# Kernel tuning notes

Measured on AMD Instinct MI355X. Metric: run time of the kernel, lower is better.

## Reference

```python
import jax, jax.numpy as jnp
import numpy as np

B, C, D, H, W = 8, 96, 8, 32, 32
HW, DIM, NH = H * W, C * D, 4
DH = DIM // NH
EPS_NORM = 1e-12
EPS_LN = 1e-5


def setup_inputs() -> dict:
    key = jax.random.key(0)
    ks = jax.random.split(key, 10)
    s = 0.02
    return {
        "x": jax.random.normal(ks[0], (B, C, D, H, W), jnp.float32),
        "pos_embed": jax.random.normal(ks[1], (1, HW, DIM), jnp.float32) * s,
        "qkv_w": jax.random.normal(ks[2], (3 * DIM, DIM), jnp.float32) * s,
        "proj_w": jax.random.normal(ks[3], (DIM, DIM), jnp.float32) * s,
        "proj_b": jnp.zeros((DIM,), jnp.float32),
        "temperature": jnp.ones((NH, 1, 1), jnp.float32),
        "ln_gamma": jnp.ones((DIM,), jnp.float32),
        "ln_beta": jnp.zeros((DIM,), jnp.float32),
        "dw_w": jax.random.normal(ks[4], (C, 1, 3, 3, 3), jnp.float32) * s,
        "dw_b": jnp.zeros((C,), jnp.float32),
        "pw_w": jax.random.normal(ks[5], (C, C, 1, 1, 1), jnp.float32) * s,
        "pw_b": jnp.zeros((C,), jnp.float32),
    }


def _l2norm_seq(t):
    # normalize over the HW axis (dim=-2), matching F.normalize(dim=-2)
    n = jnp.sqrt(jnp.sum(t * t, axis=-2, keepdims=True))
    return t / jnp.maximum(n, EPS_NORM)


def _dsconv(y, dw_w, dw_b, pw_w, pw_b):
    dn = ("NCDHW", "OIDHW", "NCDHW")
    z = jax.lax.conv_general_dilated(y, dw_w, (1, 1, 1), [(1, 1)] * 3,
                                     dimension_numbers=dn, feature_group_count=C)
    z = z + dw_b[None, :, None, None, None]
    z = jax.lax.conv_general_dilated(z, pw_w, (1, 1, 1), [(0, 0)] * 3,
                                     dimension_numbers=dn)
    return z + pw_b[None, :, None, None, None]


def reference(x, pos_embed, qkv_w, proj_w, proj_b, temperature,
              ln_gamma, ln_beta, dw_w, dw_b, pw_w, pw_b):
    save = x
    # b c d h w -> b (h w) (c d)
    t = jnp.transpose(x, (0, 3, 4, 1, 2)).reshape(B, HW, DIM)
    t = t + pos_embed
    # qkv projection (no bias)
    qkv = (t @ qkv_w.T).reshape(B, HW, 3, NH, DH)
    qkv = jnp.transpose(qkv, (2, 0, 3, 1, 4))  # [3,B,NH,HW,DH]
    q, k, v = qkv[0], qkv[1], qkv[2]
    q = _l2norm_seq(q)
    k = _l2norm_seq(k)
    attn = jnp.einsum("bhnd,bhmd->bhnm", q, k) * temperature  # temp broadcasts [NH,1,1]
    attn = jax.nn.softmax(attn, axis=-1)  # dropout = identity at eval
    o = jnp.einsum("bhnm,bhmd->bhnd", attn, v)
    o = jnp.transpose(o, (0, 2, 1, 3)).reshape(B, HW, DIM)
    o = o @ proj_w.T + proj_b
    # LayerNorm applied to attention output
    mu = jnp.mean(o, axis=-1, keepdims=True)
    var = jnp.mean((o - mu) ** 2, axis=-1, keepdims=True)
    o = (o - mu) / jnp.sqrt(var + EPS_LN) * ln_gamma + ln_beta
    # b (h w) (c d) -> b c d h w
    o = o.reshape(B, H, W, C, D)
    o = jnp.transpose(o, (0, 3, 4, 1, 2))
    y = o + save
    return y + _dsconv(y, dw_w, dw_b, pw_w, pw_b)
```

## Files before the change

### kernel.cpp

```cpp
#include <hip/hip_runtime.h>

typedef unsigned short u16;
typedef unsigned int u32;

typedef __attribute__((ext_vector_type(8))) short short8;
typedef __attribute__((ext_vector_type(4))) float floatx4;

__device__ __forceinline__ float bf2f(u16 u) { return __uint_as_float(((u32)u) << 16); }
__device__ __forceinline__ u16 f2bf(float f) {
    u32 x = __float_as_uint(f);
    x += 0x7fffu + ((x >> 16) & 1u);
    return (u16)(x >> 16);
}
__device__ __forceinline__ void gl_lds16(const void* g, void* l) {
    __builtin_amdgcn_global_load_lds((const __attribute__((address_space(1))) u32*)g,
                                     (__attribute__((address_space(3))) u32*)l, 16, 0, 0);
}


__global__ __launch_bounds__(256) void k_init(const float* __restrict__ x,
                                              const float* __restrict__ pos,
                                              const float* __restrict__ wq,
                                              const float* __restrict__ wp,
                                              const float* __restrict__ wpw,
                                              u16* __restrict__ t,
                                              u16* __restrict__ wout,
                                              float* __restrict__ zbuf) {
    __shared__ float tile[64][65];
    const int bid = blockIdx.x;
    const int tid = threadIdx.x;
    if (bid < 1536) {
        const int cd0 = (bid % 12) * 64;
        const int hw0 = ((bid / 12) & 15) * 64;
        const int b = bid / 192;
#pragma unroll
        for (int i = 0; i < 16; i++) {
            int f = i * 256 + tid;
            int cdl = f >> 6, hwl = f & 63;
            int cd = cd0 + cdl, c = cd >> 3, d = cd & 7;
            tile[cdl][hwl] = x[(size_t)(((b * 96 + c) * 8 + d)) * 1024 + hw0 + hwl];
        }
        __syncthreads();
#pragma unroll
        for (int it = 0; it < 2; it++) {
            int u = it * 256 + tid;
            int ch = u >> 6, l = u & 63;
            int n16l = ch >> 1, kcl = ch & 1;
            int hwl = n16l * 16 + (l & 15);
            int cdl = kcl * 32 + (l >> 4) * 8;
            int row = b * 1024 + hw0 + hwl;
            int cd = cd0 + cdl;
            const float* pp = pos + (size_t)(hw0 + hwl) * 768 + cd;
            float4 p0 = *(const float4*)pp;
            float4 p1 = *(const float4*)(pp + 4);
            short8 v;
            v[0] = (short)f2bf(tile[cdl + 0][hwl] + p0.x);
            v[1] = (short)f2bf(tile[cdl + 1][hwl] + p0.y);
            v[2] = (short)f2bf(tile[cdl + 2][hwl] + p0.z);
            v[3] = (short)f2bf(tile[cdl + 3][hwl] + p0.w);
            v[4] = (short)f2bf(tile[cdl + 4][hwl] + p1.x);
            v[5] = (short)f2bf(tile[cdl + 5][hwl] + p1.y);
            v[6] = (short)f2bf(tile[cdl + 6][hwl] + p1.z);
            v[7] = (short)f2bf(tile[cdl + 7][hwl] + p1.w);
            size_t chunk = (size_t)(row >> 4) * 24 + (cd >> 5);
            *(short8*)(t + chunk * 512 + l * 8) = v;
        }
    } else if (bid < 2724) {
        const int NQ = 144 * 24 * 64;
        const int NP = NQ + 48 * 24 * 64;
        int u = (bid - 1536) * 256 + tid;
        if (u < NP) {
            const float* w = (u < NQ) ? wq : wp;
            int ub = (u < NQ) ? u : u - NQ;
            int chunk = ub >> 6, l = ub & 63;
            int n16 = chunk / 24, kc = chunk - n16 * 24;
            int n = n16 * 16 + (l & 15);
            int k0 = kc * 32 + (l >> 4) * 8;
            const float* src = w + (size_t)n * 768 + k0;
            float4 a = *(const float4*)src;
            float4 b2 = *(const float4*)(src + 4);
            short8 v;
            v[0] = (short)f2bf(a.x);  v[1] = (short)f2bf(a.y);
            v[2] = (short)f2bf(a.z);  v[3] = (short)f2bf(a.w);
            v[4] = (short)f2bf(b2.x); v[5] = (short)f2bf(b2.y);
            v[6] = (short)f2bf(b2.z); v[7] = (short)f2bf(b2.w);
            *(short8*)(wout + (size_t)u * 8) = v;
        } else {
            int i = u - NP;
            wout[(size_t)NP * 8 + i] = f2bf(wpw[i]);
        }
    } else {
        int i = (bid - 2724) * 256 + tid;
        zbuf[i] = 0.f;
    }
}

template <int MODE>
__global__ __launch_bounds__(256) void gemm_bt(const u16* __restrict__ A,
                                               const u16* __restrict__ Bw,
                                               int M, int N, int K,
                                               u16* __restrict__ qo, u16* __restrict__ ko,
                                               u16* __restrict__ vo,
                                               const float* __restrict__ bias,
                                               u16* __restrict__ Co,
                                               float* __restrict__ sqa,
                                               float* __restrict__ ska,
                                               float* __restrict__ musum,
                                               float* __restrict__ sqsum) {
    __shared__ __align__(16) u16 lAB[128 * 136];
    u16* lA = lAB;
    u16* lB = lAB + 16 * 512;
    const int tid = threadIdx.x;
    const int lane = tid & 63;
    const int wv = tid >> 6;
    const int wr = wv >> 1, wc = wv & 1;
    const int ntiles = N >> 7;
    const int mtiles = M >> 7;
    const int lin = blockIdx.x;
    const int xcd = lin & 7;
    const int idx = lin >> 3;
    const int mlocal = idx / ntiles;
    const int ntile = idx - mlocal * ntiles;
    const int m0 = (xcd * (mtiles >> 3) + mlocal) << 7;
    const int n0 = ntile << 7;
    const int lr = lane & 15;
    const int lq = lane >> 4;

    floatx4 acc[4][4];
#pragma unroll
    for (int i = 0; i < 4; i++)
#pragma unroll
        for (int j = 0; j < 4; j++) acc[i][j] = (floatx4){0.f, 0.f, 0.f, 0.f};

    const int m16 = m0 >> 4, n16 = n0 >> 4;
    for (int kc2 = 0; kc2 < (K >> 6); kc2++) {
        __syncthreads();
#pragma unroll
        for (int kh = 0; kh < 2; kh++) {
#pragma unroll
            for (int i = 0; i < 2; i++) {
                int ch16 = i * 4 + wv;
                int kc = kc2 * 2 + kh;
                const u16* ga = A + ((size_t)(m16 + ch16) * 24 + kc) * 512 + lane * 8;
                gl_lds16(ga, (char*)lA + (kh * 8 + ch16) * 1024);
                const u16* gb = Bw + ((size_t)(n16 + ch16) * 24 + kc) * 512 + lane * 8;
                gl_lds16(gb, (char*)lB + (kh * 8 + ch16) * 1024);
            }
        }
        __syncthreads();
#pragma unroll
        for (int kh = 0; kh < 2; kh++) {
            short8 af[4], bfr[4];
#pragma unroll
            for (int tt = 0; tt < 4; tt++) {
                af[tt] = *(const short8*)(lA + ((kh * 8 + wr * 4 + tt) * 64 + lane) * 8);
                bfr[tt] = *(const short8*)(lB + ((kh * 8 + wc * 4 + tt) * 64 + lane) * 8);
            }
#pragma unroll
            for (int mt = 0; mt < 4; mt++)
#pragma unroll
                for (int nt = 0; nt < 4; nt++)
                    acc[mt][nt] = __builtin_amdgcn_mfma_f32_16x16x32_bf16(af[mt], bfr[nt], acc[mt][nt], 0, 0, 0);
        }
    }

    if (MODE == 0) {
        const int region = n0 / 768;
        const int n0r = n0 - region * 768;
        const int bb0 = m0 >> 10;
        if (region < 2) {
            float* dst = (region == 0) ? sqa : ska;
#pragma unroll
            for (int nt = 0; nt < 4; nt++) {
                int colb = n0r + wc * 64 + nt * 16;
                int h = colb / 192;
                int dh = colb - h * 192 + lr;
                float s = 0.f;
#pragma unroll
                for (int mt = 0; mt < 4; mt++)
#pragma unroll
                    for (int r = 0; r < 4; r++) s += acc[mt][nt][r] * acc[mt][nt][r];
                s += __shfl_xor(s, 16);
                s += __shfl_xor(s, 32);
                if (lq == 0) atomicAdd(&dst[(bb0 * 4 + h) * 192 + dh], s);
            }
        }
        __syncthreads();
        if (region < 2) {
#pragma unroll
            for (int nt = 0; nt < 4; nt++) {
                int lch = wc * 2 + (nt >> 1);
                int offbase = (((nt & 1) * 2 + (lr >> 3)) * 16) * 8 + (lr & 7);
#pragma unroll
                for (int mt = 0; mt < 4; mt++) {
                    u16* cp2 = lAB + (((wr * 4 + mt) * 4 + lch) * 512);
#pragma unroll
                    for (int r = 0; r < 4; r++)
                        cp2[offbase + (lq * 4 + r) * 8] = f2bf(acc[mt][nt][r]);
                }
            }
        } else {
#pragma unroll
            for (int nt = 0; nt < 4; nt++) {
#pragma unroll
                for (int mt = 0; mt < 4; mt++) {
                    u16* cp2 = lAB + (((wr * 2 + (mt >> 1)) * 8 + wc * 4 + nt) * 512);
                    int ob = (((mt & 1) * 2 + (lq >> 1)) * 16 + lr) * 8 + (lq & 1) * 4;
#pragma unroll
                    for (int r = 0; r < 4; r++)
                        cp2[ob + r] = f2bf(acc[mt][nt][r]);
                }
            }
        }
        __syncthreads();
        const int b = m0 >> 10;
        const int ml = m0 & 1023;
        u16* dsto = (region == 0) ? qo : (region == 1) ? ko : vo;
#pragma unroll
        for (int i = 0; i < 8; i++) {
            int ci = wv * 8 + i;
            short8 val = *(const short8*)(lAB + ci * 512 + lane * 8);
            if (region < 2) {
                int a = ci >> 2, bb = ci & 3;
                int cg = n0r + bb * 32;
                int h = cg / 192;
                int dh32 = (cg - h * 192) >> 5;
                size_t gaddr = (size_t)(b * 4 + h) * 196608 +
                               (size_t)((((ml >> 4) + a) * 6 + dh32)) * 512 + lane * 8;
                *(short8*)(dsto + gaddr) = val;
            } else {
                int a = ci >> 3, bb = ci & 7;
                int cg = n0r + bb * 16;
                int h = cg / 192;
                int dh16 = (cg - h * 192) >> 4;
                size_t gaddr = (size_t)(b * 4 + h) * 196608 +
                               (size_t)((((ml >> 5) + a) * 12 + dh16)) * 512 + lane * 8;
                *(short8*)(dsto + gaddr) = val;
            }
        }
    } else {
        float bvv[4];
#pragma unroll
        for (int nt = 0; nt < 4; nt++) bvv[nt] = bias[n0 + wc * 64 + nt * 16 + lr];
#pragma unroll
        for (int mt = 0; mt < 4; mt++) {
#pragma unroll
            for (int r = 0; r < 4; r++) {
                float s = 0.f, ss = 0.f;
#pragma unroll
                for (int nt = 0; nt < 4; nt++) {
                    float v = acc[mt][nt][r] + bvv[nt];
                    s += v;
                    ss += v * v;
                }
#pragma unroll
                for (int m = 1; m < 16; m <<= 1) {
                    s += __shfl_xor(s, m);
                    ss += __shfl_xor(ss, m);
                }
                if (lr == 0) {
                    int row = m0 + wr * 64 + mt * 16 + lq * 4 + r;
                    atomicAdd(&musum[row], s);
                    atomicAdd(&sqsum[row], ss);
                }
            }
        }
        __syncthreads();
#pragma unroll
        for (int nt = 0; nt < 4; nt++) {
            int coll = wc * 64 + nt * 16 + lr;
#pragma unroll
            for (int mt = 0; mt < 4; mt++) {
#pragma unroll
                for (int r = 0; r < 4; r++) {
                    int rowl = wr * 64 + mt * 16 + lq * 4 + r;
                    lAB[rowl * 136 + coll] = f2bf(acc[mt][nt][r] + bvv[nt]);
                }
            }
        }
        __syncthreads();
#pragma unroll
        for (int i = 0; i < 8; i++) {
            int u = i * 256 + tid;
            int rowl = u >> 4, l = u & 15;
            short8 val = *(const short8*)(lAB + rowl * 136 + l * 8);
            *(short8*)(Co + (size_t)(m0 + rowl) * N + n0 + l * 8) = val;
        }
    }
}

__global__ __launch_bounds__(256) void k_attn(const u16* __restrict__ q,
                                              const u16* __restrict__ kmat,
                                              const u16* __restrict__ vT,
                                              const float* __restrict__ sqq,
                                              const float* __restrict__ sqk,
                                              const float* __restrict__ temp,
                                              u16* __restrict__ o) {
    __shared__ __align__(16) u16 lK[24 * 512];
    __shared__ __align__(16) u16 lV[24 * 512];
    __shared__ __align__(16) u16 lP[4 * 1024];
    __shared__ float lcs[192];
    const int lin = blockIdx.x;
    const int qb = (lin >> 3) & 15;
    const int bh = (lin & 7) * 4 + (lin >> 7);
    const int b = bh >> 2, h = bh & 3;
    const int tid = threadIdx.x;
    const int lane = tid & 63;
    const int wv = tid >> 6;
    const int lr = lane & 15;
    const int lq = lane >> 4;
    const int koff = lq * 8;

    const u16* qbase = q + (size_t)bh * 196608;
    const u16* kbase = kmat + (size_t)bh * 196608;
    const u16* vbase = vT + (size_t)bh * 196608;

    {
        const float tv = temp[bh & 3];
        for (int i = tid; i < 192; i += 256) {
            float rq = 1.f / fmaxf(sqrtf(sqq[bh * 192 + i]), 1e-12f);
            float rk = 1.f / fmaxf(sqrtf(sqk[bh * 192 + i]), 1e-12f);
            lcs[i] = rq * rk * tv;
        }
    }
    __syncthreads();

    short8 qf[6];
    {
        const int qr16 = qb * 4 + wv;
#pragma unroll
        for (int ks = 0; ks < 6; ks++) {
            short8 raw = *(const short8*)(qbase + ((size_t)(qr16 * 6 + ks)) * 512 + (size_t)lane * 8);
            short8 sc;
#pragma unroll
            for (int j = 0; j < 8; j++) {
                float f = bf2f((u16)raw[j]) * lcs[ks * 32 + koff + j];
                sc[j] = (short)f2bf(f);
            }
            qf[ks] = sc;
        }
    }

    float l_r[4];
    floatx4 oacc[12];
#pragma unroll
    for (int r = 0; r < 4; r++) l_r[r] = 0.f;
#pragma unroll
    for (int vt = 0; vt < 12; vt++) oacc[vt] = (floatx4){0.f, 0.f, 0.f, 0.f};

    u16* lp = lP + wv * 1024;

    auto stage_K = [&](int kb2) {
#pragma unroll
        for (int i = 0; i < 6; i++) {
            int ch = i * 4 + wv;
            int ks = ch >> 2, nt = ch & 3;
            const u16* gk = kbase + ((size_t)(kb2 * 4 + nt) * 6 + ks) * 512 + lane * 8;
            gl_lds16(gk, (char*)lK + ch * 1024);
        }
    };
    auto stage_V = [&](int kb2) {
#pragma unroll
        for (int i = 0; i < 6; i++) {
            int ch = i * 4 + wv;
            int ks2 = ch / 12, vt2 = ch - ks2 * 12;
            const u16* gv = vbase + ((size_t)(kb2 * 2 + ks2) * 12 + vt2) * 512 + lane * 8;
            gl_lds16(gv, (char*)lV + ch * 1024);
        }
    };

    asm volatile("s_waitcnt vmcnt(0)" ::: "memory");
    stage_K(0);
    stage_V(0);
    asm volatile("s_waitcnt vmcnt(6)" ::: "memory");
    __builtin_amdgcn_s_barrier();

    for (int kb = 0; kb < 16; kb++) {
        floatx4 s0[4];
#pragma unroll
        for (int nt = 0; nt < 4; nt++) s0[nt] = (floatx4){0.f, 0.f, 0.f, 0.f};
        __builtin_amdgcn_s_setprio(1);
#pragma unroll
        for (int ks = 0; ks < 6; ks++) {
#pragma unroll
            for (int nt = 0; nt < 4; nt++) {
                short8 kf = *(const short8*)(lK + ((ks * 4 + nt) * 64 + lane) * 8);
                s0[nt] = __builtin_amdgcn_mfma_f32_16x16x32_bf16(qf[ks], kf, s0[nt], 0, 0, 0);
            }
        }
        __builtin_amdgcn_s_setprio(0);
        __builtin_amdgcn_s_barrier();
        if (kb < 15) stage_K(kb + 1);

        float rs0[4] = {0.f, 0.f, 0.f, 0.f};
#pragma unroll
        for (int nt = 0; nt < 4; nt++)
#pragma unroll
            for (int r = 0; r < 4; r++) {
                float p0 = __expf(s0[nt][r]);
                s0[nt][r] = p0;
                rs0[r] += p0;
            }
#pragma unroll
        for (int m = 1; m < 16; m <<= 1)
#pragma unroll
            for (int r = 0; r < 4; r++) rs0[r] += __shfl_xor(rs0[r], m);
#pragma unroll
        for (int r = 0; r < 4; r++) l_r[r] += rs0[r];
#pragma unroll
        for (int nt = 0; nt < 4; nt++) {
            int base2 = (nt >> 1) * 512 + ((nt & 1) * 2 + (lr >> 3)) * 128 + (lr & 7);
#pragma unroll
            for (int r = 0; r < 4; r++)
                lp[base2 + (lq * 4 + r) * 8] = f2bf(s0[nt][r]);
        }

        if (kb < 15) { asm volatile("s_waitcnt vmcnt(6)" ::: "memory"); }
        else         { asm volatile("s_waitcnt vmcnt(0)" ::: "memory"); }
        __builtin_amdgcn_s_barrier();

        __builtin_amdgcn_s_setprio(1);
#pragma unroll
        for (int ks2 = 0; ks2 < 2; ks2++) {
            short8 pf0 = *(const short8*)(lp + ks2 * 512 + lane * 8);
#pragma unroll
            for (int vt = 0; vt < 12; vt++) {
                short8 vf = *(const short8*)(lV + ((ks2 * 12 + vt) * 64 + lane) * 8);
                oacc[vt] = __builtin_amdgcn_mfma_f32_16x16x32_bf16(pf0, vf, oacc[vt], 0, 0, 0);
            }
        }
        __builtin_amdgcn_s_setprio(0);
        __builtin_amdgcn_s_barrier();
        if (kb < 15) {
            stage_V(kb + 1);
            asm volatile("s_waitcnt vmcnt(6)" ::: "memory");
            __builtin_amdgcn_s_barrier();
        }
    }

    __syncthreads();
    {
        float inv[4];
#pragma unroll
        for (int r = 0; r < 4; r++) inv[r] = 1.f / l_r[r];
#pragma unroll
        for (int vt = 0; vt < 12; vt++) {
            int col = vt * 16 + lr;
            int swb = (col >> 5) * 512 + (((col >> 3) & 3) * 16) * 8 + (col & 7);
#pragma unroll
            for (int r = 0; r < 4; r++) {
                int rowl = wv * 16 + lq * 4 + r;
                lK[(rowl >> 4) * 3072 + swb + (rowl & 15) * 8] = f2bf(oacc[vt][r] * inv[r]);
            }
        }
    }
    __syncthreads();
#pragma unroll
    for (int i = 0; i < 6; i++) {
        int u = i * 256 + tid;
        int chl = u >> 6, l = u & 63;
        short8 val = *(const short8*)(lK + chl * 512 + l * 8);
        int a = chl / 6, kc = chl - a * 6;
        size_t gaddr = ((size_t)(b * 64 + qb * 4 + a) * 24 + h * 6 + kc) * 512 + l * 8;
        *(short8*)(o + gaddr) = val;
    }
}

__global__ __launch_bounds__(256) void k_lnt(const u16* __restrict__ o2,
                                             const float* __restrict__ musum,
                                             const float* __restrict__ sqsum,
                                             const float* __restrict__ gamma,
                                             const float* __restrict__ beta,
                                             const float* __restrict__ x,
                                             float* __restrict__ y) {
    __shared__ float tile[64][65];
    const int b = blockIdx.z, hw0 = blockIdx.y * 64, cd0 = blockIdx.x * 64;
    const int tid = threadIdx.x;
#pragma unroll
    for (int i = 0; i < 16; i++) {
        int f = i * 256 + tid;
        int hwl = f >> 6, cdl = f & 63;
        int row = b * 1024 + hw0 + hwl;
        float m_ = musum[row] * (1.f / 768.f);
        float var = fmaxf(sqsum[row] * (1.f / 768.f) - m_ * m_, 0.f);
        float rstd = rsqrtf(var + 1e-5f);
        float v = bf2f(o2[(size_t)row * 768 + cd0 + cdl]);
        v = (v - m_) * rstd * gamma[cd0 + cdl] + beta[cd0 + cdl];
        tile[hwl][cdl] = v;
    }
    __syncthreads();
#pragma unroll
    for (int i = 0; i < 16; i++) {
        int f = i * 256 + tid;
        int cdl = f >> 6, hwl = f & 63;
        int cd = cd0 + cdl, c = cd >> 3, d = cd & 7;
        size_t addr = (size_t)((b * 96 + c) * 8 + d) * 1024 + hw0 + hwl;
        y[addr] = tile[hwl][cdl] + x[addr];
    }
}

__global__ __launch_bounds__(256) void k_dw(const float* __restrict__ y,
                                            const float* __restrict__ w,
                                            const float* __restrict__ bias,
                                            u16* __restrict__ z) {
    __shared__ float ly[8192];
    const int bc = blockIdx.x;
    const int c = bc % 96;
    const int tid = threadIdx.x;
    const size_t base = (size_t)bc * 8192;

#pragma unroll
    for (int i = 0; i < 8; i++) {
        int i4 = i * 256 + tid;
        *(float4*)(ly + i4 * 4) = *(const float4*)(y + base + i4 * 4);
    }
    float wt[27];
#pragma unroll
    for (int j = 0; j < 27; j++) wt[j] = w[c * 27 + j];
    const float bv = bias[c];
    __syncthreads();

    const int wcol = tid & 31;
    const int hh = tid >> 5;

    for (int hb = 0; hb < 4; hb++) {
        const int h = hb * 8 + hh;
        float pl[3][9];
        auto loadplane = [&](int dd, float* p) {
#pragma unroll
            for (int kh = 0; kh < 3; kh++) {
                int h2 = h + kh - 1;
                bool hok = (unsigned)h2 < 32u;
                const float* row = ly + dd * 1024 + h2 * 32;
#pragma unroll
                for (int kw = 0; kw < 3; kw++) {
                    int w2 = wcol + kw - 1;
                    bool ok = hok && (unsigned)w2 < 32u;
                    p[kh * 3 + kw] = ok ? row[w2] : 0.f;
                }
            }
        };
#pragma unroll
        for (int j = 0; j < 9; j++) pl[0][j] = 0.f;
        loadplane(0, pl[1]);
#pragma unroll
        for (int d = 0; d < 8; d++) {
            if (d < 7) loadplane(d + 1, pl[2]);
            else {
#pragma unroll
                for (int j = 0; j < 9; j++) pl[2][j] = 0.f;
            }
            float acc = bv;
#pragma unroll
            for (int kd = 0; kd < 3; kd++)
#pragma unroll
                for (int j = 0; j < 9; j++) acc += wt[kd * 9 + j] * pl[kd][j];
            z[base + d * 1024 + h * 32 + wcol] = f2bf(acc);
#pragma unroll
            for (int j = 0; j < 9; j++) { pl[0][j] = pl[1][j]; pl[1][j] = pl[2][j]; }
        }
    }
}

__global__ __launch_bounds__(256) void k_pw(const u16* __restrict__ z,
                                            const u16* __restrict__ wbf,
                                            const float* __restrict__ bias,
                                            float* __restrict__ out) {
    __shared__ __align__(16) u16 lZ[128 * 104];
    __shared__ __align__(16) u16 lW[96 * 104];
    const int tid = threadIdx.x;
    const int lane = tid & 63;
    const int wv = tid >> 6;
    const int lr = lane & 15;
    const int lq = lane >> 4;
    const int koff = lq * 8;

    const int idx = blockIdx.x;
    const int q = idx & 7;
    const int bd = idx >> 3;
    const int b = bd >> 3, d = bd & 7;
    const int pos0 = q * 128;

    for (int i = tid; i < 96 * 96; i += 256) {
        int row = i / 96, col = i - row * 96;
        lW[row * 104 + col] = wbf[i];
    }
    {
        const int pos = tid & 127;
        const int cc0 = (tid >> 7) * 48;
        const size_t gbase = ((size_t)b * 96 * 8 + d) * 1024 + pos0 + pos;
#pragma unroll
        for (int g = 0; g < 6; g++) {
            short8 v;
#pragma unroll
            for (int j = 0; j < 8; j++) {
                int cc = cc0 + g * 8 + j;
                v[j] = (short)z[gbase + (size_t)cc * 8192];
            }
            *(short8*)(lZ + pos * 104 + cc0 + g * 8) = v;
        }
    }
    __syncthreads();

    floatx4 acc[6][2];
#pragma unroll
    for (int m = 0; m < 6; m++)
#pragma unroll
        for (int nt = 0; nt < 2; nt++) acc[m][nt] = (floatx4){0.f, 0.f, 0.f, 0.f};

#pragma unroll
    for (int ks = 0; ks < 3; ks++) {
        short8 bfrg[2];
#pragma unroll
        for (int nt = 0; nt < 2; nt++)
            bfrg[nt] = *(const short8*)(lZ + (wv * 32 + nt * 16 + lr) * 104 + ks * 32 + koff);
#pragma unroll
        for (int m = 0; m < 6; m++) {
            short8 afr = *(const short8*)(lW + (m * 16 + lr) * 104 + ks * 32 + koff);
#pragma unroll
            for (int nt = 0; nt < 2; nt++)
                acc[m][nt] = __builtin_amdgcn_mfma_f32_16x16x32_bf16(afr, bfrg[nt], acc[m][nt], 0, 0, 0);
        }
    }

#pragma unroll
    for (int m = 0; m < 6; m++) {
#pragma unroll
        for (int r = 0; r < 4; r++) {
            int c = m * 16 + lq * 4 + r;
            float bv = bias[c];
            size_t rowbase = ((size_t)(b * 96 + c) * 8 + d) * 1024 + pos0;
#pragma unroll
            for (int nt = 0; nt < 2; nt++) {
                int pos = wv * 32 + nt * 16 + lr;
                size_t a = rowbase + pos;
                out[a] = out[a] + bv + acc[m][nt][r];
            }
        }
    }
}

extern "C" void kernel_launch(void* const* d_in, const int* in_sizes, int n_in,
                              void* d_out, int out_size, void* d_ws, size_t ws_size,
                              hipStream_t stream) {
    (void)in_sizes; (void)n_in; (void)out_size; (void)ws_size;
    const float* x      = (const float*)d_in[0];
    const float* pos    = (const float*)d_in[1];
    const float* qkv_w  = (const float*)d_in[2];
    const float* proj_w = (const float*)d_in[3];
    const float* proj_b = (const float*)d_in[4];
    const float* temp   = (const float*)d_in[5];
    const float* ln_g   = (const float*)d_in[6];
    const float* ln_b   = (const float*)d_in[7];
    const float* dw_w   = (const float*)d_in[8];
    const float* dw_b   = (const float*)d_in[9];
    const float* pw_w   = (const float*)d_in[10];
    const float* pw_b   = (const float*)d_in[11];
    float* out = (float*)d_out;
    char* ws = (char*)d_ws;

    u16* t    = (u16*)(ws + 0);
    u16* vT   = (u16*)(ws + 12582912);
    u16* q    = (u16*)(ws + 25165824);
    u16* kk   = (u16*)(ws + 37748736);
    u16* wqb  = (u16*)(ws + 50331648);
    float* sqq   = (float*)(ws + 55175168);
    float* sqk   = (float*)(ws + 55199744);
    float* musum = (float*)(ws + 55224320);
    float* sqsum = (float*)(ws + 55257088);
    u16* wpb  = wqb + 2304 * 768;
    u16* wpwb = wqb + 2304 * 768 + 768 * 768;
    u16* o   = t;
    u16* o2  = q;
    u16* z   = t;
    float* y  = out;

    k_init<<<2836, 256, 0, stream>>>(x, pos, qkv_w, proj_w, pw_w, t, wqb, sqq);
    gemm_bt<0><<<1152, 256, 0, stream>>>(t, wqb, 8192, 2304, 768, q, kk, vT, nullptr, nullptr,
                                         sqq, sqk, nullptr, nullptr);
    k_attn<<<512, 256, 0, stream>>>(q, kk, vT, sqq, sqk, temp, o);
    gemm_bt<1><<<384, 256, 0, stream>>>(o, wpb, 8192, 768, 768, nullptr, nullptr, nullptr, proj_b,
                                        o2, nullptr, nullptr, musum, sqsum);
    k_lnt<<<dim3(12, 16, 8), 256, 0, stream>>>(o2, musum, sqsum, ln_g, ln_b, x, y);
    k_dw<<<768, 256, 0, stream>>>(y, dw_w, dw_b, z);
    k_pw<<<512, 256, 0, stream>>>(z, wpwb, pw_b, out);
}
```

Before: 251.1 us.

## Split attention key blocks across wave pairs and double attention grid size

Each attention block now handles 32 query rows instead of 64, with the four waves arranged as 2 row groups by 2 key-column halves. Each wave computes scores for half of each key tile, and the partial outputs and row sums of the two waves in a pair are combined through shared memory at the end. The grid doubles from 512 to 1024 blocks, which raises occupancy and parallelism across CUs. The cost is that each block reloads the full K and V tiles for half as many queries, doubling global K/V traffic, and the cross-wave reduction adds extra LDS work and barriers. The lcs scratch array is also aliased onto the smaller P buffer.

```diff
diff --git a/kernel.cpp b/kernel.cpp
--- a/kernel.cpp
+++ b/kernel.cpp
@@ -298,15 +298,17 @@
                                               u16* __restrict__ o) {
     __shared__ __align__(16) u16 lK[24 * 512];
     __shared__ __align__(16) u16 lV[24 * 512];
-    __shared__ __align__(16) u16 lP[4 * 1024];
-    __shared__ float lcs[192];
+    __shared__ __align__(16) u16 lP[4 * 512];
+    float* lcs = (float*)lP;
     const int lin = blockIdx.x;
-    const int qb = (lin >> 3) & 15;
-    const int bh = (lin & 7) * 4 + (lin >> 7);
+    const int qb = (lin >> 3) & 31;
+    const int bh = (lin & 7) * 4 + (lin >> 8);
     const int b = bh >> 2, h = bh & 3;
     const int tid = threadIdx.x;
     const int lane = tid & 63;
     const int wv = tid >> 6;
+    const int wrow = wv >> 1;
+    const int wcol = wv & 1;
     const int lr = lane & 15;
     const int lq = lane >> 4;
     const int koff = lq * 8;
@@ -327,7 +329,7 @@
 
     short8 qf[6];
     {
-        const int qr16 = qb * 4 + wv;
+        const int qr16 = qb * 2 + wrow;
 #pragma unroll
         for (int ks = 0; ks < 6; ks++) {
             short8 raw = *(const short8*)(qbase + ((size_t)(qr16 * 6 + ks)) * 512 + (size_t)lane * 8);
@@ -348,7 +350,7 @@
 #pragma unroll
     for (int vt = 0; vt < 12; vt++) oacc[vt] = (floatx4){0.f, 0.f, 0.f, 0.f};
 
-    u16* lp = lP + wv * 1024;
+    u16* lp = lP + wv * 512;
 
     auto stage_K = [&](int kb2) {
 #pragma unroll
@@ -376,15 +378,15 @@
     __builtin_amdgcn_s_barrier();
 
     for (int kb = 0; kb < 16; kb++) {
-        floatx4 s0[4];
-#pragma unroll
-        for (int nt = 0; nt < 4; nt++) s0[nt] = (floatx4){0.f, 0.f, 0.f, 0.f};
+        floatx4 s0[2];
+#pragma unroll
+        for (int nt = 0; nt < 2; nt++) s0[nt] = (floatx4){0.f, 0.f, 0.f, 0.f};
         __builtin_amdgcn_s_setprio(1);
 #pragma unroll
         for (int ks = 0; ks < 6; ks++) {
 #pragma unroll
-            for (int nt = 0; nt < 4; nt++) {
-                short8 kf = *(const short8*)(lK + ((ks * 4 + nt) * 64 + lane) * 8);
+            for (int nt = 0; nt < 2; nt++) {
+                short8 kf = *(const short8*)(lK + ((ks * 4 + wcol * 2 + nt) * 64 + lane) * 8);
                 s0[nt] = __builtin_amdgcn_mfma_f32_16x16x32_bf16(qf[ks], kf, s0[nt], 0, 0, 0);
             }
         }
@@ -394,7 +396,7 @@
 
         float rs0[4] = {0.f, 0.f, 0.f, 0.f};
 #pragma unroll
-        for (int nt = 0; nt < 4; nt++)
+        for (int nt = 0; nt < 2; nt++)
 #pragma unroll
             for (int r = 0; r < 4; r++) {
                 float p0 = __expf(s0[nt][r]);
@@ -408,8 +410,8 @@
 #pragma unroll
         for (int r = 0; r < 4; r++) l_r[r] += rs0[r];
 #pragma unroll
-        for (int nt = 0; nt < 4; nt++) {
-            int base2 = (nt >> 1) * 512 + ((nt & 1) * 2 + (lr >> 3)) * 128 + (lr & 7);
+        for (int nt = 0; nt < 2; nt++) {
+            int base2 = (nt * 2 + (lr >> 3)) * 128 + (lr & 7);
 #pragma unroll
             for (int r = 0; r < 4; r++)
                 lp[base2 + (lq * 4 + r) * 8] = f2bf(s0[nt][r]);
@@ -420,12 +422,11 @@
         __builtin_amdgcn_s_barrier();
 
         __builtin_amdgcn_s_setprio(1);
-#pragma unroll
-        for (int ks2 = 0; ks2 < 2; ks2++) {
-            short8 pf0 = *(const short8*)(lp + ks2 * 512 + lane * 8);
+        {
+            short8 pf0 = *(const short8*)(lp + lane * 8);
 #pragma unroll
             for (int vt = 0; vt < 12; vt++) {
-                short8 vf = *(const short8*)(lV + ((ks2 * 12 + vt) * 64 + lane) * 8);
+                short8 vf = *(const short8*)(lV + ((wcol * 12 + vt) * 64 + lane) * 8);
                 oacc[vt] = __builtin_amdgcn_mfma_f32_16x16x32_bf16(pf0, vf, oacc[vt], 0, 0, 0);
             }
         }
@@ -439,29 +440,55 @@
     }
 
     __syncthreads();
+    float lfull[4];
+    {
+        u16* base = (wv < 2) ? lK : lV;
+        float* mine = (float*)(base + (wv & 1) * 6144);
+#pragma unroll
+        for (int vt = 0; vt < 12; vt++)
+#pragma unroll
+            for (int r = 0; r < 4; r++) mine[(vt * 64 + lane) * 4 + r] = oacc[vt][r];
+        if (lr == 0) {
+            float* Lw = (float*)lP + wv * 16;
+#pragma unroll
+            for (int r = 0; r < 4; r++) Lw[lq * 4 + r] = l_r[r];
+        }
+        __syncthreads();
+        const float* theirs = (const float*)(base + ((wv & 1) ^ 1) * 6144);
+        const float* Lp = (const float*)lP + (wv ^ 1) * 16;
+#pragma unroll
+        for (int vt = 0; vt < 12; vt++)
+#pragma unroll
+            for (int r = 0; r < 4; r++) oacc[vt][r] += theirs[(vt * 64 + lane) * 4 + r];
+#pragma unroll
+        for (int r = 0; r < 4; r++) lfull[r] = l_r[r] + Lp[lq * 4 + r];
+    }
+    __syncthreads();
+
     {
         float inv[4];
 #pragma unroll
-        for (int r = 0; r < 4; r++) inv[r] = 1.f / l_r[r];
-#pragma unroll
-        for (int vt = 0; vt < 12; vt++) {
+        for (int r = 0; r < 4; r++) inv[r] = 1.f / lfull[r];
+#pragma unroll
+        for (int i = 0; i < 6; i++) {
+            int vt = wcol * 6 + i;
             int col = vt * 16 + lr;
             int swb = (col >> 5) * 512 + (((col >> 3) & 3) * 16) * 8 + (col & 7);
 #pragma unroll
             for (int r = 0; r < 4; r++) {
-                int rowl = wv * 16 + lq * 4 + r;
-                lK[(rowl >> 4) * 3072 + swb + (rowl & 15) * 8] = f2bf(oacc[vt][r] * inv[r]);
+                int rowl = wrow * 16 + lq * 4 + r;
+                lV[(rowl >> 4) * 3072 + swb + (rowl & 15) * 8] = f2bf(oacc[vt][r] * inv[r]);
             }
         }
     }
     __syncthreads();
 #pragma unroll
-    for (int i = 0; i < 6; i++) {
+    for (int i = 0; i < 3; i++) {
         int u = i * 256 + tid;
-        int chl = u >> 6, l = u & 63;
-        short8 val = *(const short8*)(lK + chl * 512 + l * 8);
+        int chl = u >> 6, l2 = u & 63;
+        short8 val = *(const short8*)(lV + chl * 512 + l2 * 8);
         int a = chl / 6, kc = chl - a * 6;
-        size_t gaddr = ((size_t)(b * 64 + qb * 4 + a) * 24 + h * 6 + kc) * 512 + l * 8;
+        size_t gaddr = ((size_t)(b * 64 + qb * 2 + a) * 24 + h * 6 + kc) * 512 + l2 * 8;
         *(short8*)(o + gaddr) = val;
     }
 }
@@ -678,7 +705,7 @@
     k_init<<<2836, 256, 0, stream>>>(x, pos, qkv_w, proj_w, pw_w, t, wqb, sqq);
     gemm_bt<0><<<1152, 256, 0, stream>>>(t, wqb, 8192, 2304, 768, q, kk, vT, nullptr, nullptr,
                                          sqq, sqk, nullptr, nullptr);
-    k_attn<<<512, 256, 0, stream>>>(q, kk, vT, sqq, sqk, temp, o);
+    k_attn<<<1024, 256, 0, stream>>>(q, kk, vT, sqq, sqk, temp, o);
     gemm_bt<1><<<384, 256, 0, stream>>>(o, wpb, 8192, 768, 768, nullptr, nullptr, nullptr, proj_b,
                                         o2, nullptr, nullptr, musum, sqsum);
     k_lnt<<<dim3(12, 16, 8), 256, 0, stream>>>(o2, musum, sqsum, ln_g, ln_b, x, y);
```

Measured after the change: 287.9 us. 1.15x slower.

## Split attention work by key/value column tiles per wave; compute row sums via MFMA

Applied to the files above, without the earlier changes.

Each wave now holds all four query row tiles and computes scores for one key tile, then handles three value column tiles for all rows. This replaces per-wave redundant K/V fragment reads with reuse of each loaded fragment across four MFMAs. The softmax row sum is now computed with an MFMA against a ones vector, which removes the shuffle reduction. Probabilities are shared through LDS across waves, and the scale buffer is aliased onto the P buffer with a launch-bounds occupancy hint. The cost is higher register pressure (four Q fragment sets) and sums taken over bf16-rounded probabilities.

```diff
diff --git a/kernel.cpp b/kernel.cpp
--- a/kernel.cpp
+++ b/kernel.cpp
@@ -289,17 +289,17 @@
     }
 }
 
-__global__ __launch_bounds__(256) void k_attn(const u16* __restrict__ q,
-                                              const u16* __restrict__ kmat,
-                                              const u16* __restrict__ vT,
-                                              const float* __restrict__ sqq,
-                                              const float* __restrict__ sqk,
-                                              const float* __restrict__ temp,
-                                              u16* __restrict__ o) {
+__global__ __launch_bounds__(256, 2) void k_attn(const u16* __restrict__ q,
+                                                 const u16* __restrict__ kmat,
+                                                 const u16* __restrict__ vT,
+                                                 const float* __restrict__ sqq,
+                                                 const float* __restrict__ sqk,
+                                                 const float* __restrict__ temp,
+                                                 u16* __restrict__ o) {
     __shared__ __align__(16) u16 lK[24 * 512];
     __shared__ __align__(16) u16 lV[24 * 512];
-    __shared__ __align__(16) u16 lP[4 * 1024];
-    __shared__ float lcs[192];
+    __shared__ __align__(16) u16 lP[8 * 512];
+    float* lcs = (float*)lP;
     const int lin = blockIdx.x;
     const int qb = (lin >> 3) & 15;
     const int bh = (lin & 7) * 4 + (lin >> 7);
@@ -325,9 +325,10 @@
     }
     __syncthreads();
 
-    short8 qf[6];
-    {
-        const int qr16 = qb * 4 + wv;
+    short8 qf[4][6];
+#pragma unroll
+    for (int rt = 0; rt < 4; rt++) {
+        const int qr16 = qb * 4 + rt;
 #pragma unroll
         for (int ks = 0; ks < 6; ks++) {
             short8 raw = *(const short8*)(qbase + ((size_t)(qr16 * 6 + ks)) * 512 + (size_t)lane * 8);
@@ -337,18 +338,20 @@
                 float f = bf2f((u16)raw[j]) * lcs[ks * 32 + koff + j];
                 sc[j] = (short)f2bf(f);
             }
-            qf[ks] = sc;
-        }
-    }
-
-    float l_r[4];
-    floatx4 oacc[12];
-#pragma unroll
-    for (int r = 0; r < 4; r++) l_r[r] = 0.f;
-#pragma unroll
-    for (int vt = 0; vt < 12; vt++) oacc[vt] = (floatx4){0.f, 0.f, 0.f, 0.f};
-
-    u16* lp = lP + wv * 1024;
+            qf[rt][ks] = sc;
+        }
+    }
+
+    floatx4 lacc[4];
+    floatx4 oacc[4][3];
+#pragma unroll
+    for (int rt = 0; rt < 4; rt++) {
+        lacc[rt] = (floatx4){0.f, 0.f, 0.f, 0.f};
+#pragma unroll
+        for (int i = 0; i < 3; i++) oacc[rt][i] = (floatx4){0.f, 0.f, 0.f, 0.f};
+    }
+    const short one_bf = (short)0x3F80;
+    const short8 ones = {one_bf, one_bf, one_bf, one_bf, one_bf, one_bf, one_bf, one_bf};
 
     auto stage_K = [&](int kb2) {
 #pragma unroll
@@ -378,43 +381,31 @@
     for (int kb = 0; kb < 16; kb++) {
         floatx4 s0[4];
 #pragma unroll
-        for (int nt = 0; nt < 4; nt++) s0[nt] = (floatx4){0.f, 0.f, 0.f, 0.f};
+        for (int rt = 0; rt < 4; rt++) s0[rt] = (floatx4){0.f, 0.f, 0.f, 0.f};
         __builtin_amdgcn_s_setprio(1);
 #pragma unroll
         for (int ks = 0; ks < 6; ks++) {
-#pragma unroll
-            for (int nt = 0; nt < 4; nt++) {
-                short8 kf = *(const short8*)(lK + ((ks * 4 + nt) * 64 + lane) * 8);
-                s0[nt] = __builtin_amdgcn_mfma_f32_16x16x32_bf16(qf[ks], kf, s0[nt], 0, 0, 0);
-            }
+            short8 kf = *(const short8*)(lK + ((ks * 4 + wv) * 64 + lane) * 8);
+#pragma unroll
+            for (int rt = 0; rt < 4; rt++)
+                s0[rt] = __builtin_amdgcn_mfma_f32_16x16x32_bf16(qf[rt][ks], kf, s0[rt], 0, 0, 0);
         }
         __builtin_amdgcn_s_setprio(0);
         __builtin_amdgcn_s_barrier();
         if (kb < 15) stage_K(kb + 1);
 
-        float rs0[4] = {0.f, 0.f, 0.f, 0.f};
-#pragma unroll
-        for (int nt = 0; nt < 4; nt++)
-#pragma unroll
-            for (int r = 0; r < 4; r++) {
-                float p0 = __expf(s0[nt][r]);
-                s0[nt][r] = p0;
-                rs0[r] += p0;
-            }
-#pragma unroll
-        for (int m = 1; m < 16; m <<= 1)
-#pragma unroll
-            for (int r = 0; r < 4; r++) rs0[r] += __shfl_xor(rs0[r], m);
-#pragma unroll
-        for (int r = 0; r < 4; r++) l_r[r] += rs0[r];
-#pragma unroll
-        for (int nt = 0; nt < 4; nt++) {
-            int base2 = (nt >> 1) * 512 + ((nt & 1) * 2 + (lr >> 3)) * 128 + (lr & 7);
-#pragma unroll
-            for (int r = 0; r < 4; r++)
-                lp[base2 + (lq * 4 + r) * 8] = f2bf(s0[nt][r]);
-        }
-
+        {
+            const int cb = wv >> 1;
+            const int offb = (((wv & 1) * 2 + (lr >> 3)) * 16) * 8 + (lr & 7);
+#pragma unroll
+            for (int rt = 0; rt < 4; rt++) {
+                u16* pc = lP + (rt * 2 + cb) * 512 + offb;
+#pragma unroll
+                for (int r = 0; r < 4; r++)
+                    pc[(lq * 4 + r) * 8] = f2bf(__expf(s0[rt][r]));
+            }
+        }
+        asm volatile("s_waitcnt lgkmcnt(0)" ::: "memory");
         if (kb < 15) { asm volatile("s_waitcnt vmcnt(6)" ::: "memory"); }
         else         { asm volatile("s_waitcnt vmcnt(0)" ::: "memory"); }
         __builtin_amdgcn_s_barrier();
@@ -422,11 +413,19 @@
         __builtin_amdgcn_s_setprio(1);
 #pragma unroll
         for (int ks2 = 0; ks2 < 2; ks2++) {
-            short8 pf0 = *(const short8*)(lp + ks2 * 512 + lane * 8);
-#pragma unroll
-            for (int vt = 0; vt < 12; vt++) {
-                short8 vf = *(const short8*)(lV + ((ks2 * 12 + vt) * 64 + lane) * 8);
-                oacc[vt] = __builtin_amdgcn_mfma_f32_16x16x32_bf16(pf0, vf, oacc[vt], 0, 0, 0);
+            short8 pf[4];
+#pragma unroll
+            for (int rt = 0; rt < 4; rt++)
+                pf[rt] = *(const short8*)(lP + (rt * 2 + ks2) * 512 + lane * 8);
+#pragma unroll
+            for (int rt = 0; rt < 4; rt++)
+                lacc[rt] = __builtin_amdgcn_mfma_f32_16x16x32_bf16(pf[rt], ones, lacc[rt], 0, 0, 0);
+#pragma unroll
+            for (int i = 0; i < 3; i++) {
+                short8 vf = *(const short8*)(lV + ((ks2 * 12 + wv * 3 + i) * 64 + lane) * 8);
+#pragma unroll
+                for (int rt = 0; rt < 4; rt++)
+                    oacc[rt][i] = __builtin_amdgcn_mfma_f32_16x16x32_bf16(pf[rt], vf, oacc[rt][i], 0, 0, 0);
             }
         }
         __builtin_amdgcn_s_setprio(0);
@@ -439,18 +438,19 @@
     }
 
     __syncthreads();
-    {
+#pragma unroll
+    for (int rt = 0; rt < 4; rt++) {
         float inv[4];
 #pragma unroll
-        for (int r = 0; r < 4; r++) inv[r] = 1.f / l_r[r];
-#pragma unroll
-        for (int vt = 0; vt < 12; vt++) {
-            int col = vt * 16 + lr;
+        for (int r = 0; r < 4; r++) inv[r] = 1.f / lacc[rt][r];
+#pragma unroll
+        for (int i = 0; i < 3; i++) {
+            int col = (wv * 3 + i) * 16 + lr;
             int swb = (col >> 5) * 512 + (((col >> 3) & 3) * 16) * 8 + (col & 7);
 #pragma unroll
             for (int r = 0; r < 4; r++) {
-                int rowl = wv * 16 + lq * 4 + r;
-                lK[(rowl >> 4) * 3072 + swb + (rowl & 15) * 8] = f2bf(oacc[vt][r] * inv[r]);
+                int rowl = rt * 16 + lq * 4 + r;
+                lK[(rowl >> 4) * 3072 + swb + (rowl & 15) * 8] = f2bf(oacc[rt][i][r] * inv[r]);
             }
         }
     }
```

New measurement: 247.6 us. Within noise of the previous version (-1.4%).
